# Performance work log

Hardware: AMD Instinct MI355X
Metric: run time of the kernel (lower is better)

## Reference

```python
import jax, jax.numpy as jnp
import numpy as np

N = 2_000_000
IN_DIM = 1
HID = 64
NUM_SEG = 2048


def setup_inputs() -> dict:
    key = jax.random.key(0)
    ks = jax.random.split(key, 8)
    x = jax.random.normal(ks[0], (N, IN_DIM), dtype=jnp.float32)
    batch = jnp.sort(jax.random.randint(ks[1], (N,), 0, NUM_SEG, dtype=jnp.int64))
    s1 = 1.0 / np.sqrt(IN_DIM)
    s2 = 1.0 / np.sqrt(HID)
    W1 = jax.random.uniform(ks[2], (HID, IN_DIM), jnp.float32, -s1, s1)
    b1 = jax.random.uniform(ks[3], (HID,), jnp.float32, -s1, s1)
    W2 = jax.random.uniform(ks[4], (HID, HID), jnp.float32, -s2, s2)
    b2 = jax.random.uniform(ks[5], (HID,), jnp.float32, -s2, s2)
    W3 = jax.random.uniform(ks[6], (1, HID), jnp.float32, -s2, s2)
    b3 = jax.random.uniform(ks[7], (1,), jnp.float32, -s2, s2)
    return {"x": x, "batch": batch, "W1": W1, "b1": b1, "W2": W2, "b2": b2, "W3": W3, "b3": b3}


def reference(x, batch, W1, b1, W2, b2, W3, b3):
    batch = batch.astype(jnp.int32)
    h = jax.nn.relu(x @ W1.T + b1)          # [N, HID]
    h = jax.nn.relu(h @ W2.T + b2)          # [N, HID]
    pooled = jax.ops.segment_sum(h, batch, num_segments=NUM_SEG)  # [NUM_SEG, HID]
    counts = jax.ops.segment_sum(jnp.ones((h.shape[0],), h.dtype), batch, num_segments=NUM_SEG)
    pooled = pooled / jnp.maximum(counts, 1.0)[:, None]  # segment mean
    weights = jax.nn.relu((pooled @ W3.T + b3)[:, 0])    # [NUM_SEG]
    return weights[batch]                    # broadcast back to points [N]
```

## Files before the change

### kernel.cpp

```cpp
#include <hip/hip_runtime.h>
#include <math.h>

#define NSEG 2048
#define ROW 65
#define MMAX 4226
#define TCAP 4240
#define NC 4096
#define GLO (-9.0f)
#define GHI (9.0f)
#define DXF ((GHI - GLO) / NC)
#define INVDX (NC / (GHI - GLO))
#define SCAN_PPT 8

__global__ __launch_bounds__(256) void k_pre_scan(
    const float* __restrict__ W1, const float* __restrict__ b1,
    const float* __restrict__ W2, const float* __restrict__ b2,
    const float* __restrict__ W3, const int* __restrict__ batch,
    float* __restrict__ bpg, float* __restrict__ knots, float2* __restrict__ coef,
    int* __restrict__ nvalid, int* __restrict__ seg_start, int* __restrict__ seg_end,
    int n)
{
    __shared__ float bps[64];
    __shared__ float w2s[64 * 65];
    __shared__ float sc_[64], sda[64], sdb[64];
    const int tid = threadIdx.x;

    if (blockIdx.x >= 65) {
        int bid2 = blockIdx.x - 65;
        int base = bid2 * (256 * SCAN_PPT) + tid * SCAN_PPT;
        if (base >= n) return;
        const int4* bp = (const int4*)(batch + base);
        int4 a4 = bp[0], b4 = bp[1];
        int ss[SCAN_PPT] = {a4.x, a4.y, a4.z, a4.w, b4.x, b4.y, b4.z, b4.w};
        int prev = (base > 0) ? batch[base - 1] : -1;
#pragma unroll
        for (int p = 0; p < SCAN_PPT; ++p) {
            int u = (p == 0) ? prev : ss[p - 1];
            int v = ss[p];
            if (v != u) {
                int i = base + p;
                for (int s = (u > 0 ? u : 0); s < v; ++s) seg_end[s] = i;
                for (int s = u + 1; s <= v; ++s) seg_start[s] = i;
            }
        }
        if (base + SCAN_PPT >= n) {
            int u = ss[SCAN_PPT - 1];
            for (int s = u; s < NSEG; ++s) seg_end[s] = n;
            for (int s = u + 1; s < NSEG; ++s) seg_start[s] = n;
        }
        return;
    }

    const int k = blockIdx.x;
    const int lane = tid & 63;

    if (tid < 64) {
        float w1l = W1[lane], b1l = b1[lane];
        float t = (w1l != 0.0f) ? (-b1l / w1l) : 3.0e38f;
        int r = 0;
        for (int l = 0; l < 64; ++l) {
            float o = __shfl(t, l);
            r += (o < t) || (o == t && l < lane);
        }
        bps[r] = t;
    }
    for (int i = tid; i < 4096; i += 256)
        w2s[(i >> 6) * 65 + (i & 63)] = W2[i];
    __syncthreads();
    if (k == 0 && tid < 64) bpg[lane] = bps[lane];

    float a0 = 0.0f, b0 = 0.0f;
    if (tid < 64) {
        float lof = (k == 0) ? (bps[0] - 1.0f) : bps[k - 1];
        float hif = (k == 64) ? (bps[63] + 1.0f) : bps[k];
        float xm = lof + 0.5f * (hif - lof);
        float a = 0.0f, b = b2[lane];
        for (int j = 0; j < 64; ++j) {
            float w1 = W1[j];
            if (w1 * xm + b1[j] > 0.0f) {
                float w2 = w2s[lane * 65 + j];
                a += w2 * w1;
                b += w2 * b1[j];
            }
        }

        float w3 = W3[lane];
        float lo = (k == 0) ? -INFINITY : bps[k - 1];
        float hi = (k == 64) ? INFINITY : bps[k];
        float c = INFINITY, da = 0.0f, db = 0.0f;
        if (a != 0.0f) {
            float cc = -b / a;
            if (cc > lo && cc < hi) {
                float s = (a > 0.0f) ? 1.0f : -1.0f;
                c = cc; da = s * w3 * a; db = s * w3 * b;
            }
        }
        bool act;
        if (k == 0) act = (a < 0.0f) || (a == 0.0f && b > 0.0f);
        else { float v = a * lo + b; act = (v > 0.0f) || (v == 0.0f && a > 0.0f); }
        a0 = act ? w3 * a : 0.0f;
        b0 = act ? w3 * b : 0.0f;
        for (int d = 32; d; d >>= 1) { a0 += __shfl_xor(a0, d); b0 += __shfl_xor(b0, d); }

        int rank = 0;
        for (int l = 0; l < 64; ++l) {
            float o = __shfl(c, l);
            rank += (o < c) || (o == c && l < lane);
        }
        sc_[rank] = c; sda[rank] = da; sdb[rank] = db;
    }
    __syncthreads();
    if (tid < 64) {
        float cs = sc_[lane], das = sda[lane], dbs = sdb[lane];
        for (int d = 1; d < 64; d <<= 1) {
            float ta = __shfl_up(das, d);
            float tb = __shfl_up(dbs, d);
            if (lane >= d) { das += ta; dbs += tb; }
        }
        knots[k * ROW + lane] = cs;
        if (lane == 0) coef[k * ROW] = make_float2(a0, b0);
        coef[k * ROW + lane + 1] = make_float2(a0 + das, b0 + dbs);

        unsigned long long vm = __ballot(isfinite(cs));
        if (lane == 0) nvalid[k] = (int)__popcll(vm);
    }
}

__global__ __launch_bounds__(64) void k_pre_c2(
    const float* __restrict__ bpg, const int* __restrict__ nvalid,
    const float* __restrict__ knots2d, const float2* __restrict__ coef2d,
    float* __restrict__ Tf, float2* __restrict__ Cf,
    unsigned short* __restrict__ baseg, int* __restrict__ Mg)
{
    const int lane = threadIdx.x;
    const int k = blockIdx.x;
    __shared__ float bps[64];
    __shared__ float trow[64];

    bps[lane] = bpg[lane];
    trow[lane] = knots2d[k * ROW + lane];

    int v = nvalid[lane] + 1;
    int sc = v;
    for (int d = 1; d < 64; d <<= 1) {
        int tt = __shfl_up(sc, d);
        if (lane >= d) sc += tt;
    }
    const int offk  = (k == 0) ? 0 : __shfl(sc, k - 1);
    const int off64 = __shfl(sc, 63);
    const int nv    = nvalid[k];
    __syncthreads();

    for (int j = lane; j <= nv; j += 64) {
        if (j < nv) Tf[offk + j] = trow[j];
        else if (k < 64) Tf[offk + j] = bps[k];
        Cf[offk + j] = coef2d[k * ROW + j];
    }
    if (k == 64) {
        const int M = off64 + nvalid[64];
        float2 lastC = coef2d[64 * ROW + nvalid[64]];
        for (int i = M + lane; i < TCAP; i += 64) Tf[i] = INFINITY;
        for (int i = M + 1 + lane; i < MMAX; i += 64) Cf[i] = lastC;
        if (lane == 0) Mg[0] = M;
    }

    float lob = (k == 0) ? GLO : bps[k - 1];
    float hib = (k == 64) ? GHI : bps[k];
    float clo = fminf(fmaxf((lob - GLO) * INVDX, 0.0f), (float)(NC - 1));
    float chi = fminf(fmaxf((hib - GLO) * INVDX, 0.0f), (float)(NC - 1));
    int c0 = max(0, (int)clo - 1);
    int c1 = min(NC - 1, (int)chi + 1);
    for (int c = c0 + lane; c <= c1; c += 64) {
        float left = GLO + c * DXF;
        bool ok = (k == 0 || left >= bps[k - 1]) && (k == 64 || left < bps[k]);
        if (ok) {
            int j = 0;
#pragma unroll
            for (int ofs = 32; ofs >= 1; ofs >>= 1)
                if (trow[j + ofs - 1] <= left) j += ofs;
            if (j < 64 && trow[j] <= left) ++j;
            baseg[c] = (unsigned short)(offk + j);
        }
    }
}

__global__ __launch_bounds__(256) void k_eval_out(
    const float* __restrict__ x,
    const int* __restrict__ seg_start, const int* __restrict__ seg_end,
    const float* __restrict__ Tf, const float2* __restrict__ Cf,
    const unsigned short* __restrict__ baseg, const int* __restrict__ Mg,
    const float* __restrict__ b3, float* __restrict__ out)
{
    __shared__ __align__(16) float T_s[TCAP];
    __shared__ double wsum[4];
    __shared__ float w_s;
    const int tid = threadIdx.x;
    const int s = blockIdx.x;

    const int stageN = min(TCAP, (Mg[0] + 32) & ~15);
    for (int i = tid; i < (stageN >> 2); i += 256)
        ((float4*)T_s)[i] = ((const float4*)Tf)[i];

    const int start = seg_start[s];
    const int end   = seg_end[s];
    __syncthreads();
    if (start >= end) return;

    double acc = 0.0;
    for (int i = start + tid; i < end; i += 256) {
        float xv = x[i];
        int m;
        if (xv >= GLO) {
            int c = (int)((xv - GLO) * INVDX);
            c = c < NC - 1 ? c : NC - 1;
            if (c > 0 && GLO + c * DXF > xv) --c;
            int b0i = baseg[c];
            int a0 = b0i & ~3;
            const float4* tw = (const float4*)(T_s + a0);
            float4 t0 = tw[0], t1 = tw[1], t2 = tw[2];
            int cw = (t0.x <= xv) + (t0.y <= xv) + (t0.z <= xv) + (t0.w <= xv)
                   + (t1.x <= xv) + (t1.y <= xv) + (t1.z <= xv) + (t1.w <= xv)
                   + (t2.x <= xv) + (t2.y <= xv) + (t2.z <= xv) + (t2.w <= xv);
            m = a0 + cw;
            if (cw == 12) { while (T_s[m] <= xv) ++m; }
        } else m = 0;
        float2 ab = Cf[m];
        acc += (double)fmaf(ab.x, xv, ab.y);
    }

    for (int d = 32; d; d >>= 1) acc += __shfl_down(acc, d);
    if ((tid & 63) == 0) wsum[tid >> 6] = acc;
    __syncthreads();
    if (tid == 0) {
        double tot = wsum[0] + wsum[1] + wsum[2] + wsum[3];
        double mean = tot / (double)(end - start);
        w_s = fmaxf((float)(mean + (double)b3[0]), 0.0f);
    }
    __syncthreads();
    const float w = w_s;
    for (int i = start + tid; i < end; i += 256) out[i] = w;
}

extern "C" void kernel_launch(void* const* d_in, const int* in_sizes, int n_in,
                              void* d_out, int out_size, void* d_ws, size_t ws_size,
                              hipStream_t stream)
{
    const float* x   = (const float*)d_in[0];
    const int* batch = (const int*)d_in[1];
    const float* W1 = (const float*)d_in[2];
    const float* b1 = (const float*)d_in[3];
    const float* W2 = (const float*)d_in[4];
    const float* b2 = (const float*)d_in[5];
    const float* W3 = (const float*)d_in[6];
    const float* b3 = (const float*)d_in[7];
    float* out = (float*)d_out;
    const int n = in_sizes[0];

    char* ws = (char*)d_ws;
    int*    seg_start= (int*)ws;
    int*    seg_end  = (int*)(ws + 8192);
    float*  bpg      = (float*)(ws + 16384);
    int*    nvalid   = (int*)(ws + 16640);
    int*    Mg       = (int*)(ws + 16912);
    float*  knots2d  = (float*)(ws + 16928);
    float2* coef2d   = (float2*)(ws + 33840);
    float*  Tflat    = (float*)(ws + 67648);
    float2* Cflat    = (float2*)(ws + 84608);
    unsigned short* baseg = (unsigned short*)(ws + 118416);

    const int scanBlocks = (n + 256 * SCAN_PPT - 1) / (256 * SCAN_PPT);
    k_pre_scan<<<65 + scanBlocks, 256, 0, stream>>>(
        W1, b1, W2, b2, W3, batch, bpg, knots2d, coef2d, nvalid,
        seg_start, seg_end, n);
    k_pre_c2<<<65, 64, 0, stream>>>(bpg, nvalid, knots2d, coef2d,
                                    Tflat, Cflat, baseg, Mg);
    k_eval_out<<<NSEG, 256, 0, stream>>>(x, seg_start, seg_end, Tflat, Cflat,
                                         baseg, Mg, b3, out);
}
```

Baseline: 30.02 us.

## Drop flattening kernel and use two-level binary search over 2D knot table

```diff
diff --git a/kernel.cpp b/kernel.cpp
--- a/kernel.cpp
+++ b/kernel.cpp
@@ -3,13 +3,7 @@
 
 #define NSEG 2048
 #define ROW 65
-#define MMAX 4226
-#define TCAP 4240
-#define NC 4096
-#define GLO (-9.0f)
-#define GHI (9.0f)
-#define DXF ((GHI - GLO) / NC)
-#define INVDX (NC / (GHI - GLO))
+#define N2D (65 * ROW)
 #define SCAN_PPT 8
 
 __global__ __launch_bounds__(256) void k_pre_scan(
@@ -17,8 +11,7 @@
     const float* __restrict__ W2, const float* __restrict__ b2,
     const float* __restrict__ W3, const int* __restrict__ batch,
     float* __restrict__ bpg, float* __restrict__ knots, float2* __restrict__ coef,
-    int* __restrict__ nvalid, int* __restrict__ seg_start, int* __restrict__ seg_end,
-    int n)
+    int* __restrict__ seg_start, int* __restrict__ seg_end, int n)
 {
     __shared__ float bps[64];
     __shared__ float w2s[64 * 65];
@@ -120,111 +113,46 @@
         knots[k * ROW + lane] = cs;
         if (lane == 0) coef[k * ROW] = make_float2(a0, b0);
         coef[k * ROW + lane + 1] = make_float2(a0 + das, b0 + dbs);
-
-        unsigned long long vm = __ballot(isfinite(cs));
-        if (lane == 0) nvalid[k] = (int)__popcll(vm);
-    }
-}
-
-__global__ __launch_bounds__(64) void k_pre_c2(
-    const float* __restrict__ bpg, const int* __restrict__ nvalid,
-    const float* __restrict__ knots2d, const float2* __restrict__ coef2d,
-    float* __restrict__ Tf, float2* __restrict__ Cf,
-    unsigned short* __restrict__ baseg, int* __restrict__ Mg)
-{
-    const int lane = threadIdx.x;
-    const int k = blockIdx.x;
-    __shared__ float bps[64];
-    __shared__ float trow[64];
-
-    bps[lane] = bpg[lane];
-    trow[lane] = knots2d[k * ROW + lane];
-
-    int v = nvalid[lane] + 1;
-    int sc = v;
-    for (int d = 1; d < 64; d <<= 1) {
-        int tt = __shfl_up(sc, d);
-        if (lane >= d) sc += tt;
-    }
-    const int offk  = (k == 0) ? 0 : __shfl(sc, k - 1);
-    const int off64 = __shfl(sc, 63);
-    const int nv    = nvalid[k];
-    __syncthreads();
-
-    for (int j = lane; j <= nv; j += 64) {
-        if (j < nv) Tf[offk + j] = trow[j];
-        else if (k < 64) Tf[offk + j] = bps[k];
-        Cf[offk + j] = coef2d[k * ROW + j];
-    }
-    if (k == 64) {
-        const int M = off64 + nvalid[64];
-        float2 lastC = coef2d[64 * ROW + nvalid[64]];
-        for (int i = M + lane; i < TCAP; i += 64) Tf[i] = INFINITY;
-        for (int i = M + 1 + lane; i < MMAX; i += 64) Cf[i] = lastC;
-        if (lane == 0) Mg[0] = M;
-    }
-
-    float lob = (k == 0) ? GLO : bps[k - 1];
-    float hib = (k == 64) ? GHI : bps[k];
-    float clo = fminf(fmaxf((lob - GLO) * INVDX, 0.0f), (float)(NC - 1));
-    float chi = fminf(fmaxf((hib - GLO) * INVDX, 0.0f), (float)(NC - 1));
-    int c0 = max(0, (int)clo - 1);
-    int c1 = min(NC - 1, (int)chi + 1);
-    for (int c = c0 + lane; c <= c1; c += 64) {
-        float left = GLO + c * DXF;
-        bool ok = (k == 0 || left >= bps[k - 1]) && (k == 64 || left < bps[k]);
-        if (ok) {
-            int j = 0;
-#pragma unroll
-            for (int ofs = 32; ofs >= 1; ofs >>= 1)
-                if (trow[j + ofs - 1] <= left) j += ofs;
-            if (j < 64 && trow[j] <= left) ++j;
-            baseg[c] = (unsigned short)(offk + j);
-        }
     }
 }
 
 __global__ __launch_bounds__(256) void k_eval_out(
     const float* __restrict__ x,
     const int* __restrict__ seg_start, const int* __restrict__ seg_end,
-    const float* __restrict__ Tf, const float2* __restrict__ Cf,
-    const unsigned short* __restrict__ baseg, const int* __restrict__ Mg,
+    const float* __restrict__ bpg, const float* __restrict__ knots2d,
+    const float2* __restrict__ coef2d,
     const float* __restrict__ b3, float* __restrict__ out)
 {
-    __shared__ __align__(16) float T_s[TCAP];
+    __shared__ float bps_s[64];
+    __shared__ float T2_s[N2D];
     __shared__ double wsum[4];
     __shared__ float w_s;
     const int tid = threadIdx.x;
     const int s = blockIdx.x;
 
-    const int stageN = min(TCAP, (Mg[0] + 32) & ~15);
-    for (int i = tid; i < (stageN >> 2); i += 256)
-        ((float4*)T_s)[i] = ((const float4*)Tf)[i];
-
     const int start = seg_start[s];
     const int end   = seg_end[s];
+
+    if (tid < 64) bps_s[tid] = bpg[tid];
+    for (int i = tid; i < N2D; i += 256) T2_s[i] = knots2d[i];
     __syncthreads();
     if (start >= end) return;
 
     double acc = 0.0;
     for (int i = start + tid; i < end; i += 256) {
         float xv = x[i];
-        int m;
-        if (xv >= GLO) {
-            int c = (int)((xv - GLO) * INVDX);
-            c = c < NC - 1 ? c : NC - 1;
-            if (c > 0 && GLO + c * DXF > xv) --c;
-            int b0i = baseg[c];
-            int a0 = b0i & ~3;
-            const float4* tw = (const float4*)(T_s + a0);
-            float4 t0 = tw[0], t1 = tw[1], t2 = tw[2];
-            int cw = (t0.x <= xv) + (t0.y <= xv) + (t0.z <= xv) + (t0.w <= xv)
-                   + (t1.x <= xv) + (t1.y <= xv) + (t1.z <= xv) + (t1.w <= xv)
-                   + (t2.x <= xv) + (t2.y <= xv) + (t2.z <= xv) + (t2.w <= xv);
-            m = a0 + cw;
-            if (cw == 12) { while (T_s[m] <= xv) ++m; }
-        } else m = 0;
-        float2 ab = Cf[m];
+        int k = 0;
+#pragma unroll
+        for (int ofs = 32; ofs >= 1; ofs >>= 1)
+            if (bps_s[k + ofs - 1] <= xv) k += ofs;
+        k += (k < 64 && bps_s[k] <= xv) ? 1 : 0;
+        const int kb = k * ROW;
+        int j = 0;
+#pragma unroll
+        for (int ofs = 32; ofs >= 1; ofs >>= 1)
+            if (T2_s[kb + j + ofs - 1] <= xv) j += ofs;
+        j += (j < 64 && T2_s[kb + j] <= xv) ? 1 : 0;
+        float2 ab = coef2d[kb + j];
         acc += (double)fmaf(ab.x, xv, ab.y);
     }
 
@@ -260,20 +188,13 @@
     int*    seg_start= (int*)ws;
     int*    seg_end  = (int*)(ws + 8192);
     float*  bpg      = (float*)(ws + 16384);
-    int*    nvalid   = (int*)(ws + 16640);
-    int*    Mg       = (int*)(ws + 16912);
-    float*  knots2d  = (float*)(ws + 16928);
-    float2* coef2d   = (float2*)(ws + 33840);
-    float*  Tflat    = (float*)(ws + 67648);
-    float2* Cflat    = (float2*)(ws + 84608);
-    unsigned short* baseg = (unsigned short*)(ws + 118416);
+    float*  knots2d  = (float*)(ws + 16640);
+    float2* coef2d   = (float2*)(ws + 33552);
 
     const int scanBlocks = (n + 256 * SCAN_PPT - 1) / (256 * SCAN_PPT);
     k_pre_scan<<<65 + scanBlocks, 256, 0, stream>>>(
-        W1, b1, W2, b2, W3, batch, bpg, knots2d, coef2d, nvalid,
+        W1, b1, W2, b2, W3, batch, bpg, knots2d, coef2d,
         seg_start, seg_end, n);
-    k_pre_c2<<<65, 64, 0, stream>>>(bpg, nvalid, knots2d, coef2d,
-                                    Tflat, Cflat, baseg, Mg);
-    k_eval_out<<<NSEG, 256, 0, stream>>>(x, seg_start, seg_end, Tflat, Cflat,
-                                         baseg, Mg, b3, out);
+    k_eval_out<<<NSEG, 256, 0, stream>>>(x, seg_start, seg_end, bpg,
+                                         knots2d, coef2d, b3, out);
 }
```

Measured after the change: 27.04 us. 9.9% less time.
